# Kernel optimization log

Hardware: AMD Instinct MI355X
Metric: run time of the kernel (lower is better)

The kernel has to match this reference:

```python
import jax, jax.numpy as jnp
import numpy as np

N_EMBD = 1024
N_HEAD = 16
HEAD_DIM = N_EMBD // N_HEAD
B, T = 2, 2048


def setup_inputs() -> dict:
    key = jax.random.key(0)
    ks = jax.random.split(key, 9)
    s = 1.0 / np.sqrt(N_EMBD)
    return {
        "x": jax.random.normal(ks[0], (B, T, N_EMBD), dtype=jnp.float32),
        "Wq": jax.random.normal(ks[1], (N_EMBD, N_EMBD), dtype=jnp.float32) * s,
        "bq": jax.random.normal(ks[2], (N_EMBD,), dtype=jnp.float32) * s,
        "Wk": jax.random.normal(ks[3], (N_EMBD, N_EMBD), dtype=jnp.float32) * s,
        "bk": jax.random.normal(ks[4], (N_EMBD,), dtype=jnp.float32) * s,
        "Wv": jax.random.normal(ks[5], (N_EMBD, N_EMBD), dtype=jnp.float32) * s,
        "bv": jax.random.normal(ks[6], (N_EMBD,), dtype=jnp.float32) * s,
        "Wp": jax.random.normal(ks[7], (N_EMBD, N_EMBD), dtype=jnp.float32) * s,
        "bp": jax.random.normal(ks[8], (N_EMBD,), dtype=jnp.float32) * s,
    }


def reference(x, Wq, bq, Wk, bk, Wv, bv, Wp, bp):
    b, t, c = x.shape
    # torch Linear: y = x @ W.T + b
    def proj(W, bias):
        y = jnp.einsum('btc,oc->bto', x, W) + bias
        return y.reshape(b, t, N_HEAD, HEAD_DIM).transpose(0, 2, 1, 3)  # [B,H,T,D]

    q = proj(Wq, bq)
    k = proj(Wk, bk)
    v = proj(Wv, bv)

    scale = 1.0 / np.sqrt(HEAD_DIM).astype(np.float32)
    scores = jnp.einsum('bhqd,bhkd->bhqk', q, k) * scale  # [B,H,T,T]
    causal = jnp.tril(jnp.ones((t, t), dtype=bool))
    scores = jnp.where(causal[None, None], scores, jnp.float32(-jnp.inf))
    attn = jax.nn.softmax(scores, axis=-1)
    out = jnp.einsum('bhqk,bhkd->bhqd', attn, v)  # [B,H,T,D]
    out = out.transpose(0, 2, 1, 3).reshape(b, t, c)
    out = jnp.einsum('btc,oc->bto', out, Wp) + bp
    return out
```

## Files before the change

kernel.cpp:

```cpp
#include <hip/hip_runtime.h>
#include <hip/hip_bf16.h>

#define TT 2048
#define MM 4096
#define KS_LD 72

typedef __attribute__((ext_vector_type(8))) short bf16x8;
typedef __attribute__((ext_vector_type(4))) float f32x4;

__device__ inline short f2bf(float f){
  union { float f; unsigned u; } x; x.f = f;
  unsigned r = x.u + 0x7FFFu + ((x.u >> 16) & 1u);
  return (short)(r >> 16);
}

__device__ inline void async16(const void* g, void* l){
  __builtin_amdgcn_global_load_lds((const __attribute__((address_space(1))) void*)g,
                                   (__attribute__((address_space(3))) void*)l, 16, 0, 0);
}

__global__ void cvt_all(const float* __restrict__ x,
                        const float* __restrict__ Wq, const float* __restrict__ Wk,
                        const float* __restrict__ Wv, const float* __restrict__ Wp,
                        short* __restrict__ xb, short* __restrict__ Wqb, short* __restrict__ Wkb,
                        short* __restrict__ Wvb, short* __restrict__ Wpb){
  int b = blockIdx.x;
  const float* in; short* out; int base;
  if (b < 4096)      { in = x;  out = xb;  base = b; }
  else if (b < 5120) { in = Wq; out = Wqb; base = b - 4096; }
  else if (b < 6144) { in = Wk; out = Wkb; base = b - 5120; }
  else if (b < 7168) { in = Wv; out = Wvb; base = b - 6144; }
  else               { in = Wp; out = Wpb; base = b - 7168; }
  int i = base * 256 + threadIdx.x;
  float4 v = ((const float4*)in)[i];
  short4 o;
  o.x = f2bf(v.x); o.y = f2bf(v.y); o.z = f2bf(v.z); o.w = f2bf(v.w);
  ((short4*)out)[i] = o;
}

__device__ inline void gemm_core(const short* __restrict__ A, const short* __restrict__ Wm,
                                 short* As, short* Bs, int m0, int n0,
                                 int tid, int wm, int wn, int quad, int lr,
                                 f32x4 acc[4][4])
{
  const int row = tid >> 2, col = (tid & 3) << 3;
  const short* Ap0 = A  + (size_t)(m0 + row) * 1024 + col;
  const short* Ap1 = A  + (size_t)(m0 + row + 64) * 1024 + col;
  const short* Bp0 = Wm + (size_t)(n0 + row) * 1024 + col;
  const short* Bp1 = Wm + (size_t)(n0 + row + 64) * 1024 + col;
  for (int kt = 0; kt < 32; ++kt){
    const int kk = kt * 32;
    async16(Ap0 + kk, As + (size_t)tid * 8);
    async16(Ap1 + kk, As + (size_t)(tid + 256) * 8);
    async16(Bp0 + kk, Bs + (size_t)tid * 8);
    async16(Bp1 + kk, Bs + (size_t)(tid + 256) * 8);
    __syncthreads();
    bf16x8 aF[4], bF[4];
#pragma unroll
    for (int mt = 0; mt < 4; ++mt) aF[mt] = *(const bf16x8*)(As + (wm*64 + mt*16 + lr)*32 + quad*8);
#pragma unroll
    for (int nt = 0; nt < 4; ++nt) bF[nt] = *(const bf16x8*)(Bs + (wn*64 + nt*16 + lr)*32 + quad*8);
#pragma unroll
    for (int mt = 0; mt < 4; ++mt)
#pragma unroll
      for (int nt = 0; nt < 4; ++nt)
        acc[mt][nt] = __builtin_amdgcn_mfma_f32_16x16x32_bf16(aF[mt], bF[nt], acc[mt][nt], 0, 0, 0);
    __syncthreads();
  }
}

__launch_bounds__(256, 3)
__global__ void gemm_qkv(const short* __restrict__ A,
                         const short* __restrict__ W0, const short* __restrict__ W1, const short* __restrict__ W2,
                         const float* __restrict__ b0, const float* __restrict__ b1, const float* __restrict__ b2,
                         short* __restrict__ Qo, short* __restrict__ Ko, short* __restrict__ Vt)
{
  __shared__ __align__(16) short smem[9216];
  short* As = smem;
  short* Bs = smem + 4096;
  const int z = blockIdx.z;
  const short* Wm   = (z == 0) ? W0 : ((z == 1) ? W1 : W2);
  const float* bias = (z == 0) ? b0 : ((z == 1) ? b1 : b2);
  const int tid = threadIdx.x;
  const int lane = tid & 63, wave = tid >> 6;
  const int wm = wave >> 1, wn = wave & 1;
  const int quad = lane >> 4, lr = lane & 15;
  const int m0 = blockIdx.y * 128, n0 = blockIdx.x * 128;

  f32x4 acc[4][4];
#pragma unroll
  for (int i = 0; i < 4; ++i)
#pragma unroll
    for (int j = 0; j < 4; ++j)
#pragma unroll
      for (int r = 0; r < 4; ++r) acc[i][j][r] = 0.f;

  gemm_core(A, Wm, As, Bs, m0, n0, tid, wm, wn, quad, lr, acc);

  const float qscale = 0.125f * 1.4426950408889634f;
  const int bB = m0 >> 11, t0 = m0 & 2047;

  if (z == 2){
#pragma unroll
    for (int nh = 0; nh < 2; ++nh){
      __syncthreads();
      if (wn == nh){
#pragma unroll
        for (int nt = 0; nt < 4; ++nt){
          int n = n0 + wn*64 + nt*16 + lr;
          float bv = bias[n];
          int n_l = nt*16 + lr;
#pragma unroll
          for (int mt = 0; mt < 4; ++mt)
#pragma unroll
            for (int r = 0; r < 4; ++r){
              int m_l = wm*64 + mt*16 + quad*4 + r;
              smem[n_l*136 + m_l] = f2bf(acc[mt][nt][r] + bv);
            }
        }
      }
      __syncthreads();
#pragma unroll
      for (int i = 0; i < 4; ++i){
        int c = tid + i*256;
        int rowN = c >> 4, ch = c & 15;
        int4 v = *(const int4*)(smem + rowN*136 + ch*8);
        int n = n0 + nh*64 + rowN;
        int hH = n >> 6, d = n & 63;
        *(int4*)(Vt + ((size_t)((bB<<4) + hH)*64 + d)*2048 + t0 + ch*8) = v;
      }
    }
    return;
  }

  short* dst = (z == 0) ? Qo : Ko;
#pragma unroll
  for (int nh = 0; nh < 2; ++nh){
    __syncthreads();
    if (wn == nh){
#pragma unroll
      for (int nt = 0; nt < 4; ++nt){
        int n_l = nt*16 + lr;
        float bv = bias[n0 + nh*64 + n_l];
#pragma unroll
        for (int mt = 0; mt < 4; ++mt){
#pragma unroll
          for (int r = 0; r < 4; ++r){
            int m_l = wm*64 + mt*16 + quad*4 + r;
            float v = acc[mt][nt][r] + bv;
            if (z == 0) v *= qscale;
            smem[m_l*72 + n_l] = f2bf(v);
          }
        }
      }
    }
    __syncthreads();
    const int hH = (n0 + nh*64) >> 6;
    short* dhead = dst + (size_t)((bB<<4) + hH) * 2048 * 64;
#pragma unroll
    for (int i = 0; i < 4; ++i){
      int c = tid + i*256;
      int rowm = c >> 3, ch = (c & 7) << 3;
      int4 v = *(const int4*)(smem + rowm*72 + ch);
      *(int4*)(dhead + (size_t)(t0 + rowm)*64 + ch) = v;
    }
  }
}

__launch_bounds__(256, 2)
__global__ void gemm_proj(const short* __restrict__ A, const short* __restrict__ Wm,
                          const float* __restrict__ bias, float* __restrict__ out)
{
  __shared__ __align__(16) short As[128*32];
  __shared__ __align__(16) short Bs[64*32];
  const int tid = threadIdx.x;
  const int lane = tid & 63, wave = tid >> 6;
  const int quad = lane >> 4, lr = lane & 15;
  const int m0 = blockIdx.y * 128, n0 = blockIdx.x * 64;

  const int row = tid >> 2, col = (tid & 3) << 3;
  const short* Ap0 = A  + (size_t)(m0 + row) * 1024 + col;
  const short* Ap1 = A  + (size_t)(m0 + row + 64) * 1024 + col;
  const short* Bp0 = Wm + (size_t)(n0 + row) * 1024 + col;

  f32x4 acc[2][4];
#pragma unroll
  for (int i = 0; i < 2; ++i)
#pragma unroll
    for (int j = 0; j < 4; ++j)
#pragma unroll
      for (int r = 0; r < 4; ++r) acc[i][j][r] = 0.f;

  for (int kt = 0; kt < 32; ++kt){
    const int kk = kt * 32;
    async16(Ap0 + kk, As + (size_t)tid * 8);
    async16(Ap1 + kk, As + (size_t)(tid + 256) * 8);
    if (row < 64) async16(Bp0 + kk, Bs + (size_t)tid * 8);
    __syncthreads();
    bf16x8 aF[2], bF[4];
#pragma unroll
    for (int mt = 0; mt < 2; ++mt) aF[mt] = *(const bf16x8*)(As + (wave*32 + mt*16 + lr)*32 + quad*8);
#pragma unroll
    for (int nt = 0; nt < 4; ++nt) bF[nt] = *(const bf16x8*)(Bs + (nt*16 + lr)*32 + quad*8);
#pragma unroll
    for (int mt = 0; mt < 2; ++mt)
#pragma unroll
      for (int nt = 0; nt < 4; ++nt)
        acc[mt][nt] = __builtin_amdgcn_mfma_f32_16x16x32_bf16(aF[mt], bF[nt], acc[mt][nt], 0, 0, 0);
    __syncthreads();
  }

#pragma unroll
  for (int nt = 0; nt < 4; ++nt){
    int n = n0 + nt*16 + lr;
    float bv = bias[n];
#pragma unroll
    for (int mt = 0; mt < 2; ++mt){
      int mBase = m0 + wave*32 + mt*16 + quad*4;
#pragma unroll
      for (int r = 0; r < 4; ++r){
        int m = mBase + r;
        out[(size_t)m * 1024 + n] = acc[mt][nt][r] + bv;
      }
    }
  }
}

__launch_bounds__(256, 4)
__global__ void attn_kernel(const short* __restrict__ Q, const short* __restrict__ K,
                            const short* __restrict__ Vt, short* __restrict__ AO)
{
  __shared__ __align__(16) short Ks[64*KS_LD];
  __shared__ __align__(16) short Vs[64*KS_LD];
  __shared__ __align__(16) short Ps[4*16*KS_LD];
  const int tid = threadIdx.x, lane = tid & 63, wave = tid >> 6;
  const int quad = lane >> 4, lr = lane & 15;
  const int bid = blockIdx.x;
  const int qt = 31 - (bid >> 5);
  const int hb = bid & 31;
  const int bidx = hb >> 4, h = hb & 15;
  const int q0 = qt * 64;
  const int wq = q0 + wave * 16;
  const short* Qh = Q  + (size_t)hb * TT * 64;
  const short* Kh = K  + (size_t)hb * TT * 64;
  const short* Vh = Vt + (size_t)hb * 64 * TT;
  short* Pw = Ps + wave * 16 * KS_LD;

  bf16x8 qf[2];
#pragma unroll
  for (int ks = 0; ks < 2; ++ks)
    qf[ks] = *(const bf16x8*)(Qh + (size_t)(wq + lr) * 64 + ks*32 + quad*8);

  f32x4 acc_o[4], l_acc;
#pragma unroll
  for (int r = 0; r < 4; ++r) l_acc[r] = 0.f;
#pragma unroll
  for (int dt = 0; dt < 4; ++dt)
#pragma unroll
    for (int r = 0; r < 4; ++r) acc_o[dt][r] = 0.f;

  const short one_bf = (short)0x3F80;
  const bf16x8 onesf = { one_bf, one_bf, one_bf, one_bf, one_bf, one_bf, one_bf, one_bf };

  const int srow = tid >> 3, scol = (tid & 7) << 3;

  const int nkv = qt + 1;
  for (int kv = 0; kv < nkv; ++kv){
    const int kv0 = kv * 64;
    __syncthreads();
#pragma unroll
    for (int s = 0; s < 2; ++s){
      *(int4*)(Ks + (srow + s*32) * KS_LD + scol) = *(const int4*)(Kh + (size_t)(kv0 + srow + s*32) * 64 + scol);
      *(int4*)(Vs + (srow + s*32) * KS_LD + scol) = *(const int4*)(Vh + (size_t)(srow + s*32) * TT + kv0 + scol);
    }
    __syncthreads();
    if (kv0 > wq + 15) continue;

    f32x4 s4[4];
#pragma unroll
    for (int nt = 0; nt < 4; ++nt)
#pragma unroll
      for (int r = 0; r < 4; ++r) s4[nt][r] = 0.f;
#pragma unroll
    for (int nt = 0; nt < 4; ++nt)
#pragma unroll
      for (int ks = 0; ks < 2; ++ks){
        bf16x8 kf = *(const bf16x8*)(Ks + (nt*16 + lr)*KS_LD + ks*32 + quad*8);
        s4[nt] = __builtin_amdgcn_mfma_f32_16x16x32_bf16(qf[ks], kf, s4[nt], 0, 0, 0);
      }

    const bool need_mask = (kv == nkv - 1);
    const int prow = quad * 4;
    const int qg = wq + prow;
#pragma unroll
    for (int nt = 0; nt < 4; ++nt){
      const int key = kv0 + nt*16 + lr;
      float pv[4];
#pragma unroll
      for (int r = 0; r < 4; ++r){
        float v = exp2f(s4[nt][r]);
        if (need_mask && key > qg + r) v = 0.f;
        pv[r] = v;
      }
#pragma unroll
      for (int rp = 0; rp < 2; ++rp){
        __hip_bfloat162 h2 = __float22bfloat162_rn(make_float2(pv[2*rp], pv[2*rp+1]));
        unsigned u = *(unsigned*)&h2;
        Pw[(prow + 2*rp    )*KS_LD + nt*16 + lr] = (short)(u & 0xffffu);
        Pw[(prow + 2*rp + 1)*KS_LD + nt*16 + lr] = (short)(u >> 16);
      }
    }

#pragma unroll
    for (int ks = 0; ks < 2; ++ks){
      bf16x8 pf = *(const bf16x8*)(Pw + lr*KS_LD + ks*32 + quad*8);
      l_acc = __builtin_amdgcn_mfma_f32_16x16x32_bf16(pf, onesf, l_acc, 0, 0, 0);
#pragma unroll
      for (int dt = 0; dt < 4; ++dt){
        bf16x8 vf = *(const bf16x8*)(Vs + (dt*16 + lr)*KS_LD + ks*32 + quad*8);
        acc_o[dt] = __builtin_amdgcn_mfma_f32_16x16x32_bf16(pf, vf, acc_o[dt], 0, 0, 0);
      }
    }
  }

  float inv[4];
#pragma unroll
  for (int r = 0; r < 4; ++r) inv[r] = __builtin_amdgcn_rcpf(l_acc[r]);
#pragma unroll
  for (int dt = 0; dt < 4; ++dt){
    int d = dt*16 + lr;
#pragma unroll
    for (int r = 0; r < 4; ++r){
      int qg = wq + quad*4 + r;
      AO[(size_t)(bidx*2048 + qg)*1024 + h*64 + d] = f2bf(acc_o[dt][r] * inv[r]);
    }
  }
}

extern "C" void kernel_launch(void* const* d_in, const int* in_sizes, int n_in,
                              void* d_out, int out_size, void* d_ws, size_t ws_size,
                              hipStream_t stream)
{
  const float* x  = (const float*)d_in[0];
  const float* Wq = (const float*)d_in[1];
  const float* bq = (const float*)d_in[2];
  const float* Wk = (const float*)d_in[3];
  const float* bk = (const float*)d_in[4];
  const float* Wv = (const float*)d_in[5];
  const float* bv = (const float*)d_in[6];
  const float* Wp = (const float*)d_in[7];
  const float* bp = (const float*)d_in[8];
  float* out = (float*)d_out;

  char* ws = (char*)d_ws;
  const size_t MB = 1024ull * 1024ull;
  short* Qb  = (short*)(ws + 0);
  short* Kb  = (short*)(ws + 8*MB);
  short* Vtb = (short*)(ws + 16*MB);
  short* AOb = (short*)(ws + 24*MB);
  short* xb  = (short*)(ws + 32*MB);
  short* Wqb = (short*)(ws + 40*MB);
  short* Wkb = (short*)(ws + 42*MB);
  short* Wvb = (short*)(ws + 44*MB);
  short* Wpb = (short*)(ws + 46*MB);

  cvt_all<<<8192, 256, 0, stream>>>(x, Wq, Wk, Wv, Wp, xb, Wqb, Wkb, Wvb, Wpb);
  gemm_qkv<<<dim3(8, 32, 3), 256, 0, stream>>>(xb, Wqb, Wkb, Wvb, bq, bk, bv, Qb, Kb, Vtb);
  attn_kernel<<<1024, 256, 0, stream>>>(Qb, Kb, Vtb, AOb);
  gemm_proj<<<dim3(16, 32), 256, 0, stream>>>(AOb, Wpb, bp, out);
}
```

Measured before the change: 188.9 us.

## Split long causal attention rows across blocks, pair short tiles, deepen GEMM K-step

Attention work is rebalanced. The 16 longest query tiles per head are split into two KV halves whose partial outputs and row sums are combined with atomics into fp32 buffers and normalized in a new combine kernel. Short tiles are paired so each block does similar work. The QKV and projection GEMMs now load 64-wide K slices per barrier, halving the number of sync points at the cost of double the LDS. This adds a memset, atomics and an extra launch, and the x bf16 buffer now aliases the AO buffer.

```diff
diff --git a/kernel.cpp b/kernel.cpp
--- a/kernel.cpp
+++ b/kernel.cpp
@@ -43,28 +43,34 @@
                                  int tid, int wm, int wn, int quad, int lr,
                                  f32x4 acc[4][4])
 {
-  const int row = tid >> 2, col = (tid & 3) << 3;
-  const short* Ap0 = A  + (size_t)(m0 + row) * 1024 + col;
-  const short* Ap1 = A  + (size_t)(m0 + row + 64) * 1024 + col;
-  const short* Bp0 = Wm + (size_t)(n0 + row) * 1024 + col;
-  const short* Bp1 = Wm + (size_t)(n0 + row + 64) * 1024 + col;
-  for (int kt = 0; kt < 32; ++kt){
-    const int kk = kt * 32;
-    async16(Ap0 + kk, As + (size_t)tid * 8);
-    async16(Ap1 + kk, As + (size_t)(tid + 256) * 8);
-    async16(Bp0 + kk, Bs + (size_t)tid * 8);
-    async16(Bp1 + kk, Bs + (size_t)(tid + 256) * 8);
-    __syncthreads();
-    bf16x8 aF[4], bF[4];
-#pragma unroll
-    for (int mt = 0; mt < 4; ++mt) aF[mt] = *(const bf16x8*)(As + (wm*64 + mt*16 + lr)*32 + quad*8);
-#pragma unroll
-    for (int nt = 0; nt < 4; ++nt) bF[nt] = *(const bf16x8*)(Bs + (wn*64 + nt*16 + lr)*32 + quad*8);
-#pragma unroll
-    for (int mt = 0; mt < 4; ++mt)
-#pragma unroll
-      for (int nt = 0; nt < 4; ++nt)
-        acc[mt][nt] = __builtin_amdgcn_mfma_f32_16x16x32_bf16(aF[mt], bF[nt], acc[mt][nt], 0, 0, 0);
+  const int prow = tid >> 2, pcol = (tid & 3) << 3;
+  const short* Ap0 = A  + (size_t)(m0 + prow) * 1024 + pcol;
+  const short* Ap1 = A  + (size_t)(m0 + prow + 64) * 1024 + pcol;
+  const short* Bp0 = Wm + (size_t)(n0 + prow) * 1024 + pcol;
+  const short* Bp1 = Wm + (size_t)(n0 + prow + 64) * 1024 + pcol;
+  for (int kt = 0; kt < 16; ++kt){
+    const int kk = kt * 64;
+#pragma unroll
+    for (int pn = 0; pn < 2; ++pn){
+      async16(Ap0 + kk + pn*32, As + pn*4096 + (size_t)tid * 8);
+      async16(Ap1 + kk + pn*32, As + pn*4096 + (size_t)(tid + 256) * 8);
+      async16(Bp0 + kk + pn*32, Bs + pn*4096 + (size_t)tid * 8);
+      async16(Bp1 + kk + pn*32, Bs + pn*4096 + (size_t)(tid + 256) * 8);
+    }
+    __syncthreads();
+#pragma unroll
+    for (int ks = 0; ks < 2; ++ks){
+      bf16x8 aF[4], bF[4];
+#pragma unroll
+      for (int mt = 0; mt < 4; ++mt) aF[mt] = *(const bf16x8*)(As + ks*4096 + (wm*64 + mt*16 + lr)*32 + quad*8);
+#pragma unroll
+      for (int nt = 0; nt < 4; ++nt) bF[nt] = *(const bf16x8*)(Bs + ks*4096 + (wn*64 + nt*16 + lr)*32 + quad*8);
+#pragma unroll
+      for (int mt = 0; mt < 4; ++mt)
+#pragma unroll
+        for (int nt = 0; nt < 4; ++nt)
+          acc[mt][nt] = __builtin_amdgcn_mfma_f32_16x16x32_bf16(aF[mt], bF[nt], acc[mt][nt], 0, 0, 0);
+    }
     __syncthreads();
   }
 }
@@ -75,9 +81,9 @@
                          const float* __restrict__ b0, const float* __restrict__ b1, const float* __restrict__ b2,
                          short* __restrict__ Qo, short* __restrict__ Ko, short* __restrict__ Vt)
 {
-  __shared__ __align__(16) short smem[9216];
+  __shared__ __align__(16) short smem[16384];
   short* As = smem;
-  short* Bs = smem + 4096;
+  short* Bs = smem + 8192;
   const int z = blockIdx.z;
   const short* Wm   = (z == 0) ? W0 : ((z == 1) ? W1 : W2);
   const float* bias = (z == 0) ? b0 : ((z == 1) ? b1 : b2);
@@ -171,17 +177,17 @@
 __global__ void gemm_proj(const short* __restrict__ A, const short* __restrict__ Wm,
                           const float* __restrict__ bias, float* __restrict__ out)
 {
-  __shared__ __align__(16) short As[128*32];
-  __shared__ __align__(16) short Bs[64*32];
+  __shared__ __align__(16) short As[2*4096];
+  __shared__ __align__(16) short Bs[2*2048];
   const int tid = threadIdx.x;
   const int lane = tid & 63, wave = tid >> 6;
   const int quad = lane >> 4, lr = lane & 15;
   const int m0 = blockIdx.y * 128, n0 = blockIdx.x * 64;
 
-  const int row = tid >> 2, col = (tid & 3) << 3;
-  const short* Ap0 = A  + (size_t)(m0 + row) * 1024 + col;
-  const short* Ap1 = A  + (size_t)(m0 + row + 64) * 1024 + col;
-  const short* Bp0 = Wm + (size_t)(n0 + row) * 1024 + col;
+  const int prow = tid >> 2, pcol = (tid & 3) << 3;
+  const short* Ap0 = A  + (size_t)(m0 + prow) * 1024 + pcol;
+  const short* Ap1 = A  + (size_t)(m0 + prow + 64) * 1024 + pcol;
+  const short* Bp0 = Wm + (size_t)(n0 + (tid >> 2)) * 1024 + pcol;
 
   f32x4 acc[2][4];
 #pragma unroll
@@ -191,22 +197,28 @@
 #pragma unroll
       for (int r = 0; r < 4; ++r) acc[i][j][r] = 0.f;
 
-  for (int kt = 0; kt < 32; ++kt){
-    const int kk = kt * 32;
-    async16(Ap0 + kk, As + (size_t)tid * 8);
-    async16(Ap1 + kk, As + (size_t)(tid + 256) * 8);
-    if (row < 64) async16(Bp0 + kk, Bs + (size_t)tid * 8);
-    __syncthreads();
-    bf16x8 aF[2], bF[4];
-#pragma unroll
-    for (int mt = 0; mt < 2; ++mt) aF[mt] = *(const bf16x8*)(As + (wave*32 + mt*16 + lr)*32 + quad*8);
-#pragma unroll
-    for (int nt = 0; nt < 4; ++nt) bF[nt] = *(const bf16x8*)(Bs + (nt*16 + lr)*32 + quad*8);
-#pragma unroll
-    for (int mt = 0; mt < 2; ++mt)
-#pragma unroll
-      for (int nt = 0; nt < 4; ++nt)
-        acc[mt][nt] = __builtin_amdgcn_mfma_f32_16x16x32_bf16(aF[mt], bF[nt], acc[mt][nt], 0, 0, 0);
+  for (int kt = 0; kt < 16; ++kt){
+    const int kk = kt * 64;
+#pragma unroll
+    for (int pn = 0; pn < 2; ++pn){
+      async16(Ap0 + kk + pn*32, As + pn*4096 + (size_t)tid * 8);
+      async16(Ap1 + kk + pn*32, As + pn*4096 + (size_t)(tid + 256) * 8);
+      async16(Bp0 + kk + pn*32, Bs + pn*2048 + (size_t)tid * 8);
+    }
+    __syncthreads();
+#pragma unroll
+    for (int ks = 0; ks < 2; ++ks){
+      bf16x8 aF[2], bF[4];
+#pragma unroll
+      for (int mt = 0; mt < 2; ++mt) aF[mt] = *(const bf16x8*)(As + ks*4096 + (wave*32 + mt*16 + lr)*32 + quad*8);
+#pragma unroll
+      for (int nt = 0; nt < 4; ++nt) bF[nt] = *(const bf16x8*)(Bs + ks*2048 + (nt*16 + lr)*32 + quad*8);
+#pragma unroll
+      for (int mt = 0; mt < 2; ++mt)
+#pragma unroll
+        for (int nt = 0; nt < 4; ++nt)
+          acc[mt][nt] = __builtin_amdgcn_mfma_f32_16x16x32_bf16(aF[mt], bF[nt], acc[mt][nt], 0, 0, 0);
+    }
     __syncthreads();
   }
 
@@ -226,9 +238,10 @@
   }
 }
 
-__launch_bounds__(256, 4)
+__launch_bounds__(256, 5)
 __global__ void attn_kernel(const short* __restrict__ Q, const short* __restrict__ K,
-                            const short* __restrict__ Vt, short* __restrict__ AO)
+                            const short* __restrict__ Vt, short* __restrict__ AO,
+                            float* __restrict__ OAcc, float* __restrict__ lAcc)
 {
   __shared__ __align__(16) short Ks[64*KS_LD];
   __shared__ __align__(16) short Vs[64*KS_LD];
@@ -236,105 +249,164 @@
   const int tid = threadIdx.x, lane = tid & 63, wave = tid >> 6;
   const int quad = lane >> 4, lr = lane & 15;
   const int bid = blockIdx.x;
-  const int qt = 31 - (bid >> 5);
+  const int slot = bid >> 5;
   const int hb = bid & 31;
   const int bidx = hb >> 4, h = hb & 15;
-  const int q0 = qt * 64;
-  const int wq = q0 + wave * 16;
   const short* Qh = Q  + (size_t)hb * TT * 64;
   const short* Kh = K  + (size_t)hb * TT * 64;
   const short* Vh = Vt + (size_t)hb * 64 * TT;
   short* Pw = Ps + wave * 16 * KS_LD;
 
-  bf16x8 qf[2];
-#pragma unroll
-  for (int ks = 0; ks < 2; ++ks)
-    qf[ks] = *(const bf16x8*)(Qh + (size_t)(wq + lr) * 64 + ks*32 + quad*8);
-
-  f32x4 acc_o[4], l_acc;
-#pragma unroll
-  for (int r = 0; r < 4; ++r) l_acc[r] = 0.f;
-#pragma unroll
-  for (int dt = 0; dt < 4; ++dt)
-#pragma unroll
-    for (int r = 0; r < 4; ++r) acc_o[dt][r] = 0.f;
+  int qts[2], k0s[2], k1s[2], np;
+  bool partial;
+  if (slot < 32){
+    int qt = 31 - (slot >> 1);
+    int half = (qt + 1) >> 1;
+    int c = slot & 1;
+    qts[0] = qt; k0s[0] = c ? half : 0; k1s[0] = c ? (qt + 1) : half;
+    np = 1; partial = true;
+  } else {
+    int p = slot - 32;
+    qts[0] = p;      k0s[0] = 0; k1s[0] = p + 1;
+    qts[1] = 15 - p; k0s[1] = 0; k1s[1] = 16 - p;
+    np = 2; partial = false;
+  }
 
   const short one_bf = (short)0x3F80;
   const bf16x8 onesf = { one_bf, one_bf, one_bf, one_bf, one_bf, one_bf, one_bf, one_bf };
-
   const int srow = tid >> 3, scol = (tid & 7) << 3;
 
-  const int nkv = qt + 1;
-  for (int kv = 0; kv < nkv; ++kv){
-    const int kv0 = kv * 64;
-    __syncthreads();
-#pragma unroll
-    for (int s = 0; s < 2; ++s){
-      *(int4*)(Ks + (srow + s*32) * KS_LD + scol) = *(const int4*)(Kh + (size_t)(kv0 + srow + s*32) * 64 + scol);
-      *(int4*)(Vs + (srow + s*32) * KS_LD + scol) = *(const int4*)(Vh + (size_t)(srow + s*32) * TT + kv0 + scol);
-    }
-    __syncthreads();
-    if (kv0 > wq + 15) continue;
-
-    f32x4 s4[4];
-#pragma unroll
-    for (int nt = 0; nt < 4; ++nt)
-#pragma unroll
-      for (int r = 0; r < 4; ++r) s4[nt][r] = 0.f;
-#pragma unroll
-    for (int nt = 0; nt < 4; ++nt)
+  for (int ph = 0; ph < np; ++ph){
+    const int qt = qts[ph];
+    const int q0 = qt * 64;
+    const int wq = q0 + wave * 16;
+
+    bf16x8 qf[2];
+#pragma unroll
+    for (int ks = 0; ks < 2; ++ks)
+      qf[ks] = *(const bf16x8*)(Qh + (size_t)(wq + lr) * 64 + ks*32 + quad*8);
+
+    f32x4 acc_o[4], l_acc;
+#pragma unroll
+    for (int r = 0; r < 4; ++r) l_acc[r] = 0.f;
+#pragma unroll
+    for (int dt = 0; dt < 4; ++dt)
+#pragma unroll
+      for (int r = 0; r < 4; ++r) acc_o[dt][r] = 0.f;
+
+    for (int kv = k0s[ph]; kv < k1s[ph]; ++kv){
+      const int kv0 = kv * 64;
+      __syncthreads();
+#pragma unroll
+      for (int s = 0; s < 2; ++s){
+        *(int4*)(Ks + (srow + s*32) * KS_LD + scol) = *(const int4*)(Kh + (size_t)(kv0 + srow + s*32) * 64 + scol);
+        *(int4*)(Vs + (srow + s*32) * KS_LD + scol) = *(const int4*)(Vh + (size_t)(srow + s*32) * TT + kv0 + scol);
+      }
+      __syncthreads();
+      if (kv0 > wq + 15) continue;
+
+      f32x4 s4[4];
+#pragma unroll
+      for (int nt = 0; nt < 4; ++nt)
+#pragma unroll
+        for (int r = 0; r < 4; ++r) s4[nt][r] = 0.f;
+#pragma unroll
+      for (int nt = 0; nt < 4; ++nt)
+#pragma unroll
+        for (int ks = 0; ks < 2; ++ks){
+          bf16x8 kf = *(const bf16x8*)(Ks + (nt*16 + lr)*KS_LD + ks*32 + quad*8);
+          s4[nt] = __builtin_amdgcn_mfma_f32_16x16x32_bf16(qf[ks], kf, s4[nt], 0, 0, 0);
+        }
+
+      const bool need_mask = (kv0 == q0);
+      const int prow = quad * 4;
+      const int qg = wq + prow;
+#pragma unroll
+      for (int nt = 0; nt < 4; ++nt){
+        const int key = kv0 + nt*16 + lr;
+        float pv[4];
+#pragma unroll
+        for (int r = 0; r < 4; ++r){
+          float v = exp2f(s4[nt][r]);
+          if (need_mask && key > qg + r) v = 0.f;
+          pv[r] = v;
+        }
+#pragma unroll
+        for (int rp = 0; rp < 2; ++rp){
+          __hip_bfloat162 h2 = __float22bfloat162_rn(make_float2(pv[2*rp], pv[2*rp+1]));
+          unsigned u = *(unsigned*)&h2;
+          Pw[(prow + 2*rp    )*KS_LD + nt*16 + lr] = (short)(u & 0xffffu);
+          Pw[(prow + 2*rp + 1)*KS_LD + nt*16 + lr] = (short)(u >> 16);
+        }
+      }
+
 #pragma unroll
       for (int ks = 0; ks < 2; ++ks){
-        bf16x8 kf = *(const bf16x8*)(Ks + (nt*16 + lr)*KS_LD + ks*32 + quad*8);
-        s4[nt] = __builtin_amdgcn_mfma_f32_16x16x32_bf16(qf[ks], kf, s4[nt], 0, 0, 0);
-      }
-
-    const bool need_mask = (kv == nkv - 1);
-    const int prow = quad * 4;
-    const int qg = wq + prow;
-#pragma unroll
-    for (int nt = 0; nt < 4; ++nt){
-      const int key = kv0 + nt*16 + lr;
-      float pv[4];
-#pragma unroll
-      for (int r = 0; r < 4; ++r){
-        float v = exp2f(s4[nt][r]);
-        if (need_mask && key > qg + r) v = 0.f;
-        pv[r] = v;
-      }
-#pragma unroll
-      for (int rp = 0; rp < 2; ++rp){
-        __hip_bfloat162 h2 = __float22bfloat162_rn(make_float2(pv[2*rp], pv[2*rp+1]));
-        unsigned u = *(unsigned*)&h2;
-        Pw[(prow + 2*rp    )*KS_LD + nt*16 + lr] = (short)(u & 0xffffu);
-        Pw[(prow + 2*rp + 1)*KS_LD + nt*16 + lr] = (short)(u >> 16);
-      }
-    }
-
-#pragma unroll
-    for (int ks = 0; ks < 2; ++ks){
-      bf16x8 pf = *(const bf16x8*)(Pw + lr*KS_LD + ks*32 + quad*8);
-      l_acc = __builtin_amdgcn_mfma_f32_16x16x32_bf16(pf, onesf, l_acc, 0, 0, 0);
+        bf16x8 pf = *(const bf16x8*)(Pw + lr*KS_LD + ks*32 + quad*8);
+        l_acc = __builtin_amdgcn_mfma_f32_16x16x32_bf16(pf, onesf, l_acc, 0, 0, 0);
+#pragma unroll
+        for (int dt = 0; dt < 4; ++dt){
+          bf16x8 vf = *(const bf16x8*)(Vs + (dt*16 + lr)*KS_LD + ks*32 + quad*8);
+          acc_o[dt] = __builtin_amdgcn_mfma_f32_16x16x32_bf16(pf, vf, acc_o[dt], 0, 0, 0);
+        }
+      }
+    }
+
+    if (!partial){
+      float inv[4];
+#pragma unroll
+      for (int r = 0; r < 4; ++r) inv[r] = __builtin_amdgcn_rcpf(l_acc[r]);
 #pragma unroll
       for (int dt = 0; dt < 4; ++dt){
-        bf16x8 vf = *(const bf16x8*)(Vs + (dt*16 + lr)*KS_LD + ks*32 + quad*8);
-        acc_o[dt] = __builtin_amdgcn_mfma_f32_16x16x32_bf16(pf, vf, acc_o[dt], 0, 0, 0);
-      }
-    }
-  }
-
-  float inv[4];
-#pragma unroll
-  for (int r = 0; r < 4; ++r) inv[r] = __builtin_amdgcn_rcpf(l_acc[r]);
-#pragma unroll
-  for (int dt = 0; dt < 4; ++dt){
-    int d = dt*16 + lr;
-#pragma unroll
-    for (int r = 0; r < 4; ++r){
-      int qg = wq + quad*4 + r;
-      AO[(size_t)(bidx*2048 + qg)*1024 + h*64 + d] = f2bf(acc_o[dt][r] * inv[r]);
-    }
-  }
+        int d = dt*16 + lr;
+#pragma unroll
+        for (int r = 0; r < 4; ++r){
+          int qg = wq + quad*4 + r;
+          AO[(size_t)(bidx*2048 + qg)*1024 + h*64 + d] = f2bf(acc_o[dt][r] * inv[r]);
+        }
+      }
+    } else {
+      float* Ob = OAcc + (size_t)((hb*16 + (qt - 16))*64) * 64;
+#pragma unroll
+      for (int dt = 0; dt < 4; ++dt){
+        int d = dt*16 + lr;
+#pragma unroll
+        for (int r = 0; r < 4; ++r){
+          int row = wave*16 + quad*4 + r;
+          atomicAdd(Ob + (size_t)row*64 + d, acc_o[dt][r]);
+        }
+      }
+      if (lr == 0){
+        float* lb = lAcc + (hb*16 + (qt - 16))*64;
+#pragma unroll
+        for (int r = 0; r < 4; ++r)
+          atomicAdd(lb + wave*16 + quad*4 + r, l_acc[r]);
+      }
+    }
+  }
+}
+
+__global__ void attn_combine(const float* __restrict__ OAcc, const float* __restrict__ lAcc,
+                             short* __restrict__ AO)
+{
+  const int blk = blockIdx.x;
+  const int hb = blk & 31, qti = blk >> 5;
+  const int bidx = hb >> 4, h = hb & 15;
+  const int tid = threadIdx.x;
+  const int row = tid >> 2, dseg = (tid & 3) << 4;
+  const float* Op = OAcc + ((size_t)((hb*16 + qti)*64 + row)) * 64 + dseg;
+  const float inv = __builtin_amdgcn_rcpf(lAcc[(hb*16 + qti)*64 + row]);
+  float4 v0 = ((const float4*)Op)[0], v1 = ((const float4*)Op)[1];
+  float4 v2 = ((const float4*)Op)[2], v3 = ((const float4*)Op)[3];
+  short o[16];
+  o[0]=f2bf(v0.x*inv); o[1]=f2bf(v0.y*inv); o[2]=f2bf(v0.z*inv); o[3]=f2bf(v0.w*inv);
+  o[4]=f2bf(v1.x*inv); o[5]=f2bf(v1.y*inv); o[6]=f2bf(v1.z*inv); o[7]=f2bf(v1.w*inv);
+  o[8]=f2bf(v2.x*inv); o[9]=f2bf(v2.y*inv); o[10]=f2bf(v2.z*inv); o[11]=f2bf(v2.w*inv);
+  o[12]=f2bf(v3.x*inv); o[13]=f2bf(v3.y*inv); o[14]=f2bf(v3.z*inv); o[15]=f2bf(v3.w*inv);
+  const int q = 1024 + qti*64 + row;
+  short* dst = AO + (size_t)(bidx*2048 + q)*1024 + h*64 + dseg;
+  ((int4*)dst)[0] = *(const int4*)&o[0];
+  ((int4*)dst)[1] = *(const int4*)&o[8];
 }
 
 extern "C" void kernel_launch(void* const* d_in, const int* in_sizes, int n_in,
@@ -354,18 +426,23 @@
 
   char* ws = (char*)d_ws;
   const size_t MB = 1024ull * 1024ull;
-  short* Qb  = (short*)(ws + 0);
-  short* Kb  = (short*)(ws + 8*MB);
-  short* Vtb = (short*)(ws + 16*MB);
-  short* AOb = (short*)(ws + 24*MB);
-  short* xb  = (short*)(ws + 32*MB);
-  short* Wqb = (short*)(ws + 40*MB);
-  short* Wkb = (short*)(ws + 42*MB);
-  short* Wvb = (short*)(ws + 44*MB);
-  short* Wpb = (short*)(ws + 46*MB);
-
+  const size_t KB = 1024ull;
+  short* Qb   = (short*)(ws + 0);
+  short* Kb   = (short*)(ws + 8*MB);
+  short* Vtb  = (short*)(ws + 16*MB);
+  short* AOb  = (short*)(ws + 24*MB);
+  short* xb   = (short*)(ws + 24*MB);
+  float* OAcc = (float*)(ws + 32*MB);
+  float* lAcc = (float*)(ws + 40*MB);
+  short* Wqb  = (short*)(ws + 40*MB + 128*KB);
+  short* Wkb  = (short*)(ws + 42*MB + 128*KB);
+  short* Wvb  = (short*)(ws + 44*MB + 128*KB);
+  short* Wpb  = (short*)(ws + 46*MB + 128*KB);
+
+  hipMemsetAsync(ws + 32*MB, 0, 8*MB + 128*KB, stream);
   cvt_all<<<8192, 256, 0, stream>>>(x, Wq, Wk, Wv, Wp, xb, Wqb, Wkb, Wvb, Wpb);
   gemm_qkv<<<dim3(8, 32, 3), 256, 0, stream>>>(xb, Wqb, Wkb, Wvb, bq, bk, bv, Qb, Kb, Vtb);
-  attn_kernel<<<1024, 256, 0, stream>>>(Qb, Kb, Vtb, AOb);
+  attn_kernel<<<1280, 256, 0, stream>>>(Qb, Kb, Vtb, AOb, OAcc, lAcc);
+  attn_combine<<<512, 256, 0, stream>>>(OAcc, lAcc, AOb);
   gemm_proj<<<dim3(16, 32), 256, 0, stream>>>(AOb, Wpb, bp, out);
 }
```

Result: slower. 196.3 us (+3.9%).
